# Performance work log

Measured on AMD Instinct MI355X. Metric: run time of the kernel, lower is better.

The kernel has to match this reference:

```python
import jax, jax.numpy as jnp
import numpy as np

B, T, D = 64, 512, 1024   # batch, seq, input_dim
R, O = 1024, 1024          # recurrent_dim, output_dim


def setup_inputs() -> dict:
    key = jax.random.key(0)
    ks = jax.random.split(key, 8)
    s_in = 1.0 / np.sqrt(D)
    s_rec = 1.0 / np.sqrt(R)
    return {
        "x": jax.random.normal(ks[0], (B, T, D), dtype=jnp.float32),
        "Wxh": jax.random.uniform(ks[1], (R, D), jnp.float32, -s_in, s_in),
        "bh": jax.random.uniform(ks[2], (R,), jnp.float32, -s_in, s_in),
        "Whh": jax.random.uniform(ks[3], (R, R), jnp.float32, -s_rec, s_rec),
        "Wxz": jax.random.uniform(ks[4], (R, D), jnp.float32, -s_in, s_in),
        "bz": jax.random.uniform(ks[5], (R,), jnp.float32, -s_in, s_in),
        "Whz": jax.random.uniform(ks[6], (R, R), jnp.float32, -s_rec, s_rec),
        "Wy": jax.random.uniform(ks[7], (O, R), jnp.float32, -s_rec, s_rec),
        "by": jnp.zeros((O,), dtype=jnp.float32),
    }


def reference(x, Wxh, bh, Whh, Wxz, bz, Whz, Wy, by):
    # Original per-step math (note the quirk: h2z output is added to x_t
    # BEFORE x2z):
    #   z  = sigmoid(Wxz @ (x_t + Whz @ h) + bz)
    #   hb = relu(Wxh @ x_t + bh + Whh @ h)
    #   h  = z * h + (1 - z) * hb
    # Precompute all input-side GEMMs in one batched contraction (linearity);
    # fold Wxz@Whz into a single recurrent matrix.
    xh = jnp.einsum('btd,rd->btr', x, Wxh) + bh          # [B,T,R]
    xz = jnp.einsum('btd,rd->btr', x, Wxz) + bz          # [B,T,R]
    Mz = Wxz @ Whz                                        # [R,R]

    def step(h, inp):
        xh_t, xz_t = inp                                  # each [B,R]
        z = jax.nn.sigmoid(xz_t + h @ Mz.T)
        hb = jax.nn.relu(xh_t + h @ Whh.T)
        h = z * h + (1.0 - z) * hb
        return h, None

    h0 = jnp.zeros((x.shape[0], Whh.shape[0]), dtype=x.dtype)
    # scan over time: move T to leading axis
    h_final, _ = jax.lax.scan(
        step, h0, (jnp.swapaxes(xh, 0, 1), jnp.swapaxes(xz, 0, 1)))
    return h_final @ Wy.T + by                            # [B,O]
```

## Files before the change

### kernel.cpp

```cpp
#include <hip/hip_runtime.h>

#define BB 64
#define TT 512
#define DD 1024
#define RR 1024

#define SCAN_BLOCKS 32
#define HS_STRIDE 1032
#define SCAN_LDS_BYTES (64 * HS_STRIDE * 2)

typedef __bf16 bf16x8 __attribute__((ext_vector_type(8)));
typedef float f32x4 __attribute__((ext_vector_type(4)));
typedef unsigned short us4 __attribute__((ext_vector_type(4)));
typedef unsigned int u32x4 __attribute__((ext_vector_type(4)));
typedef unsigned long long u64;

__device__ inline unsigned short f2bf(float f) {
  unsigned int u = __float_as_uint(f);
  u = (u + 0x7fffu + ((u >> 16) & 1u)) >> 16;
  return (unsigned short)u;
}
__device__ inline float bf2f(unsigned short b) {
  return __uint_as_float(((unsigned int)b) << 16);
}

__device__ inline u32x4 ld16_sc(const void* p) {
  u32x4 r;
  asm volatile("global_load_dwordx4 %0, %1, off sc0 sc1"
               : "=v"(r) : "v"(p) : "memory");
  return r;
}

__global__ void k_f2b4(const float* __restrict__ in, unsigned short* __restrict__ out, int n4) {
  int i = blockIdx.x * blockDim.x + threadIdx.x;
  if (i < n4) {
    const float4 v = ((const float4*)in)[i];
    us4 o;
    o.x = f2bf(v.x); o.y = f2bf(v.y); o.z = f2bf(v.z); o.w = f2bf(v.w);
    ((us4*)out)[i] = o;
  }
}

__global__ __launch_bounds__(256) void k_transpose_bf16(
    const float* __restrict__ in, unsigned short* __restrict__ out) {
  __shared__ float tile[32][33];
  const int bx = blockIdx.x * 32, by0 = blockIdx.y * 32;
  const int tx = threadIdx.x, ty = threadIdx.y;
#pragma unroll
  for (int r = 0; r < 32; r += 8)
    tile[ty + r][tx] = in[(size_t)(by0 + ty + r) * 1024 + bx + tx];
  __syncthreads();
#pragma unroll
  for (int r = 0; r < 32; r += 8)
    out[(size_t)(bx + ty + r) * 1024 + by0 + tx] = f2bf(tile[tx][ty + r]);
}

__device__ inline void gload_lds16(const unsigned short* g, unsigned short* l) {
  __builtin_amdgcn_global_load_lds(
      (const __attribute__((address_space(1))) unsigned int*)g,
      (__attribute__((address_space(3))) unsigned int*)l, 16, 0, 0);
}

template <int EPI>
__global__ __launch_bounds__(256) void gemm_bt(
    const unsigned short* __restrict__ A,
    const unsigned short* __restrict__ Bm,
    const float* __restrict__ bias_h,
    const float* __restrict__ bias_z,
    unsigned short* __restrict__ outb, int K) {
  __shared__ __attribute__((aligned(16))) unsigned short As[128 * 32];
  __shared__ __attribute__((aligned(16))) unsigned short Bs[128 * 32];
  const int tid = threadIdx.x;
  const int m0 = blockIdx.y * 128, n0 = blockIdx.x * 128;
  const int lane = tid & 63, wid = tid >> 6;
  const int l16 = lane & 15, quad = lane >> 4;
  const int wm = (wid & 1) * 64, wn = (wid >> 1) * 64;

  f32x4 acc[4][4] = {};

  const int c0 = tid, c1 = 256 + tid;
  const int rowA0 = c0 >> 2, colA0 = (c0 & 3) << 3;
  const int rowA1 = c1 >> 2, colA1 = (c1 & 3) << 3;

  for (int kk = 0; kk < K; kk += 32) {
    __syncthreads();
    gload_lds16(A + (size_t)(m0 + rowA0) * K + kk + colA0, As + c0 * 8);
    gload_lds16(A + (size_t)(m0 + rowA1) * K + kk + colA1, As + c1 * 8);
    gload_lds16(Bm + (size_t)(n0 + rowA0) * K + kk + colA0, Bs + c0 * 8);
    gload_lds16(Bm + (size_t)(n0 + rowA1) * K + kk + colA1, Bs + c1 * 8);
    __syncthreads();
    bf16x8 af[4], bfr[4];
#pragma unroll
    for (int i = 0; i < 4; ++i) {
      af[i] = *(const bf16x8*)&As[(wm + i * 16 + l16) * 32 + quad * 8];
      bfr[i] = *(const bf16x8*)&Bs[(wn + i * 16 + l16) * 32 + quad * 8];
    }
#pragma unroll
    for (int i = 0; i < 4; ++i)
#pragma unroll
      for (int j = 0; j < 4; ++j)
        acc[i][j] = __builtin_amdgcn_mfma_f32_16x16x32_bf16(af[i], bfr[j], acc[i][j], 0, 0, 0);
  }

#pragma unroll
  for (int i = 0; i < 4; ++i) {
#pragma unroll
    for (int j = 0; j < 4; ++j) {
#pragma unroll
      for (int r = 0; r < 4; ++r) {
        const int m = m0 + wm + i * 16 + quad * 4 + r;
        const int n = n0 + wn + j * 16 + l16;
        float v = acc[i][j][r];
        if (EPI == 0) {
          v += (n < 1024) ? bias_h[n] : bias_z[n - 1024];
          const int b = m >> 9;
          const int t = m & 511;
          outb[((size_t)(t * 64 + b) << 11) + n] = f2bf(v);
        } else {
          outb[(size_t)m * 1024 + n] = f2bf(v);
        }
      }
    }
  }
}

__global__ __launch_bounds__(1024) void scan_out_k(
    const unsigned short* __restrict__ xhz,
    const unsigned short* __restrict__ Wrec,
    const unsigned short* __restrict__ Wyb,
    const float* __restrict__ by,
    unsigned short* __restrict__ hb0, unsigned short* __restrict__ hb1,
    unsigned int* __restrict__ flags,
    float* __restrict__ out) {
  extern __shared__ char smem[];
  unsigned short* hs = (unsigned short*)smem;
  float* red = (float*)smem;

  const int tid = threadIdx.x, g = blockIdx.x;
  const int lane = tid & 63, wid = tid >> 6;
  const int l16 = lane & 15, quad = lane >> 4;
  const int ks = wid >> 2, nsub = wid & 3;
  const int kw = ks * 256;
  const int i0 = g * 32;

  const int bcol = (nsub < 2) ? (i0 + nsub * 16 + l16)
                              : (1024 + i0 + (nsub - 2) * 16 + l16);
  const unsigned short* Bb = Wrec + (size_t)bcol * 1024 + kw + quad * 8;
  bf16x8 bfr[8];
#pragma unroll
  for (int s = 0; s < 8; ++s) bfr[s] = *(const bf16x8*)(Bb + s * 32);

  const int sr = tid >> 4;
  const int su = tid & 15;
  const unsigned short* gsrc_base0 = hb0 + sr * 1024 + su * 8;
  const unsigned short* gsrc_base1 = hb1 + sr * 1024 + su * 8;
  unsigned short* ldst = hs + sr * HS_STRIDE + su * 8;

  const int eb = tid >> 4, ej = (tid & 15) * 2;
  float hold0 = 0.0f, hold1 = 0.0f;

  const unsigned short* hbc = hb0;
  unsigned short* hbn = hb1;
  const unsigned short* gsrc = gsrc_base0;

  for (int tt = 0; tt < TT; ++tt) {
    u32x4 tmp[8];
#pragma unroll
    for (int c = 0; c < 8; ++c)
      tmp[c] = ld16_sc((const char*)gsrc + c * 256);
    const size_t xrow = ((size_t)(tt * 64 + eb)) << 11;
    const unsigned int xh2 = *(const unsigned int*)(xhz + xrow + i0 + ej);
    const unsigned int xz2 = *(const unsigned int*)(xhz + xrow + 1024 + i0 + ej);
    asm volatile("s_waitcnt vmcnt(0)" ::: "memory");
#pragma unroll
    for (int c = 0; c < 8; ++c)
      *(u32x4*)(ldst + c * 128) = tmp[c];
    __syncthreads();

    f32x4 acc[4] = {};
#pragma unroll
    for (int s = 0; s < 8; ++s) {
#pragma unroll
      for (int mt = 0; mt < 4; ++mt) {
        const bf16x8 afr = *(const bf16x8*)(hs + (mt * 16 + l16) * HS_STRIDE + kw + s * 32 + quad * 8);
        acc[mt] = __builtin_amdgcn_mfma_f32_16x16x32_bf16(afr, bfr[s], acc[mt], 0, 0, 0);
      }
    }
    __syncthreads();

#pragma unroll
    for (int mt = 0; mt < 4; ++mt)
#pragma unroll
      for (int r = 0; r < 4; ++r)
        red[(size_t)(ks * 64 + mt * 16 + quad * 4 + r) * 68 + nsub * 16 + l16] = acc[mt][r];
    __syncthreads();

    float ph0 = 0.f, ph1 = 0.f, pz0 = 0.f, pz1 = 0.f;
#pragma unroll
    for (int w = 0; w < 4; ++w) {
      const float* rb = red + (size_t)(w * 64 + eb) * 68;
      ph0 += rb[ej]; ph1 += rb[ej + 1];
      pz0 += rb[32 + ej]; pz1 += rb[32 + ej + 1];
    }
    {
      const float xh0 = bf2f((unsigned short)(xh2 & 0xffff));
      const float xh1 = bf2f((unsigned short)(xh2 >> 16));
      const float xz0 = bf2f((unsigned short)(xz2 & 0xffff));
      const float xz1 = bf2f((unsigned short)(xz2 >> 16));
      const float z0 = 1.0f / (1.0f + __expf(-(xz0 + pz0)));
      const float z1 = 1.0f / (1.0f + __expf(-(xz1 + pz1)));
      const float hb_0 = fmaxf(xh0 + ph0, 0.0f);
      const float hb_1 = fmaxf(xh1 + ph1, 0.0f);
      hold0 = z0 * hold0 + (1.0f - z0) * hb_0;
      hold1 = z1 * hold1 + (1.0f - z1) * hb_1;
      const unsigned int pk = (unsigned int)f2bf(hold0) | ((unsigned int)f2bf(hold1) << 16);
      __hip_atomic_store((unsigned int*)(hbn + eb * 1024 + i0 + ej), pk,
                         __ATOMIC_RELAXED, __HIP_MEMORY_SCOPE_AGENT);
    }

    __syncthreads();
    if (tid == 0)
      __hip_atomic_store(&flags[g], (unsigned int)(tt + 1),
                         __ATOMIC_RELAXED, __HIP_MEMORY_SCOPE_AGENT);
    if (tid < 64) {
      const unsigned int tgt = (unsigned int)(tt + 1);
      unsigned int v;
      do {
        v = __hip_atomic_load(&flags[tid & 31], __ATOMIC_RELAXED, __HIP_MEMORY_SCOPE_AGENT);
      } while (__any(v < tgt));
    }
    __syncthreads();

    const unsigned short* tc = hbc; hbc = hbn; hbn = (unsigned short*)tc;
    gsrc = (tt & 1) ? gsrc_base0 : gsrc_base1;
  }

  {
    u32x4 tmp[8];
#pragma unroll
    for (int c = 0; c < 8; ++c)
      tmp[c] = ld16_sc((const char*)(hbc + sr * 1024 + su * 8) + c * 256);
    asm volatile("s_waitcnt vmcnt(0)" ::: "memory");
#pragma unroll
    for (int c = 0; c < 8; ++c)
      *(u32x4*)(ldst + c * 128) = tmp[c];
  }
  __syncthreads();

  if (nsub < 2) {
    const int ocol = i0 + nsub * 16 + l16;
    const unsigned short* Byb = Wyb + (size_t)ocol * 1024 + kw + quad * 8;
    f32x4 acc[4] = {};
#pragma unroll
    for (int s = 0; s < 8; ++s) {
      const bf16x8 byf = *(const bf16x8*)(Byb + s * 32);
#pragma unroll
      for (int mt = 0; mt < 4; ++mt) {
        const bf16x8 afr = *(const bf16x8*)(hs + (mt * 16 + l16) * HS_STRIDE + kw + s * 32 + quad * 8);
        acc[mt] = __builtin_amdgcn_mfma_f32_16x16x32_bf16(afr, byf, acc[mt], 0, 0, 0);
      }
    }
    __syncthreads();
#pragma unroll
    for (int mt = 0; mt < 4; ++mt)
#pragma unroll
      for (int r = 0; r < 4; ++r)
        red[(size_t)(ks * 64 + mt * 16 + quad * 4 + r) * 68 + nsub * 16 + l16] = acc[mt][r];
  } else {
    __syncthreads();
  }
  __syncthreads();

  {
    float o0 = by[i0 + ej], o1 = by[i0 + ej + 1];
#pragma unroll
    for (int w = 0; w < 4; ++w) {
      const float* rb = red + (size_t)(w * 64 + eb) * 68;
      o0 += rb[ej]; o1 += rb[ej + 1];
    }
    float2 ov; ov.x = o0; ov.y = o1;
    *(float2*)(out + (size_t)eb * 1024 + i0 + ej) = ov;
  }
}

extern "C" void kernel_launch(void* const* d_in, const int* in_sizes, int n_in,
                              void* d_out, int out_size, void* d_ws, size_t ws_size,
                              hipStream_t stream) {
  const float* x = (const float*)d_in[0];
  const float* Wxh = (const float*)d_in[1];
  const float* bh = (const float*)d_in[2];
  const float* Whh = (const float*)d_in[3];
  const float* Wxz = (const float*)d_in[4];
  const float* bz = (const float*)d_in[5];
  const float* Whz = (const float*)d_in[6];
  const float* Wy = (const float*)d_in[7];
  const float* by = (const float*)d_in[8];
  float* out = (float*)d_out;

  char* ws = (char*)d_ws;
  size_t off = 0;
  auto alloc = [&](size_t bytes) -> void* {
    void* p = ws + off;
    off += (bytes + 255) & ~(size_t)255;
    return p;
  };
  const size_t nX = (size_t)BB * TT * DD;
  unsigned short* xb = (unsigned short*)alloc(nX * 2);
  unsigned short* Wcat = (unsigned short*)alloc((size_t)2048 * 1024 * 2);
  unsigned short* WhzT = (unsigned short*)alloc((size_t)1024 * 1024 * 2);
  unsigned short* Wrec = (unsigned short*)alloc((size_t)2048 * 1024 * 2);
  unsigned short* Wyb = (unsigned short*)alloc((size_t)1024 * 1024 * 2);
  unsigned short* xhz = (unsigned short*)alloc((size_t)TT * BB * 2048 * 2);
  unsigned short* hb0 = (unsigned short*)alloc((size_t)BB * RR * 2);
  unsigned short* hb1 = (unsigned short*)alloc((size_t)BB * RR * 2);
  unsigned int* flags = (unsigned int*)alloc(1024);

  hipMemsetAsync(hb0, 0, (size_t)BB * RR * 2, stream);
  hipMemsetAsync(flags, 0, 1024, stream);

  k_f2b4<<<dim3((unsigned)(nX / 4 / 256)), 256, 0, stream>>>(x, xb, (int)(nX / 4));
  k_f2b4<<<dim3(1024), 256, 0, stream>>>(Wxh, Wcat, 262144);
  k_f2b4<<<dim3(1024), 256, 0, stream>>>(Wxz, Wcat + 1024 * 1024, 262144);
  k_f2b4<<<dim3(1024), 256, 0, stream>>>(Whh, Wrec, 262144);
  k_f2b4<<<dim3(1024), 256, 0, stream>>>(Wy, Wyb, 262144);
  k_transpose_bf16<<<dim3(32, 32), dim3(32, 8), 0, stream>>>(Whz, WhzT);

  gemm_bt<1><<<dim3(8, 8), 256, 0, stream>>>(Wcat + 1024 * 1024, WhzT, nullptr, nullptr,
                                             Wrec + (size_t)1024 * 1024, 1024);
  gemm_bt<0><<<dim3(16, 256), 256, 0, stream>>>(xb, Wcat, bh, bz, xhz, 1024);

  hipFuncSetAttribute((const void*)scan_out_k,
                      hipFuncAttributeMaxDynamicSharedMemorySize, SCAN_LDS_BYTES);
  const unsigned short* xhz_c = xhz;
  const unsigned short* Wrec_c = Wrec;
  const unsigned short* Wyb_c = Wyb;
  const float* by_c = by;
  void* kargs[] = {(void*)&xhz_c, (void*)&Wrec_c, (void*)&Wyb_c, (void*)&by_c,
                   (void*)&hb0, (void*)&hb1, (void*)&flags, (void*)&out};
  hipLaunchCooperativeKernel((void*)scan_out_k, dim3(SCAN_BLOCKS), dim3(1024),
                             kargs, SCAN_LDS_BYTES, stream);
}
```

Measured before the change: 3.379 ms.

## Restructure recurrent scan to 64 blocks with LDS-resident weights and direct-register h loads

The persistent scan kernel moves from 32 blocks of 1024 threads to 64 blocks of 256 threads. Each block keeps its 16 h-columns and 16 z-columns of the recurrent weights in LDS, and each wave streams its 16 batch rows of h straight from global memory into MFMA operand registers, with staged waitcnt pipelining. This removes the LDS staging of h, the cross-wave K-split reduction and several block barriers per step. The flag wait moves to the start of the next step so the xhz loads overlap it. In exchange, each block reads the full h from global every step, and 64 blocks now take part in the grid-wide flag sync.

```diff
diff --git a/kernel.cpp b/kernel.cpp
--- a/kernel.cpp
+++ b/kernel.cpp
@@ -5,15 +5,16 @@
 #define DD 1024
 #define RR 1024
 
-#define SCAN_BLOCKS 32
-#define HS_STRIDE 1032
-#define SCAN_LDS_BYTES (64 * HS_STRIDE * 2)
+#define NBLK 64
+#define WST 1032
+#define SCAN_LDS_BYTES (64 * WST * 2)
+#define SCRATCH_OFF (32 * WST * 2)
 
 typedef __bf16 bf16x8 __attribute__((ext_vector_type(8)));
 typedef float f32x4 __attribute__((ext_vector_type(4)));
 typedef unsigned short us4 __attribute__((ext_vector_type(4)));
 typedef unsigned int u32x4 __attribute__((ext_vector_type(4)));
-typedef unsigned long long u64;
+typedef unsigned int u32x2 __attribute__((ext_vector_type(2)));
 
 __device__ inline unsigned short f2bf(float f) {
   unsigned int u = __float_as_uint(f);
@@ -29,6 +30,15 @@
   asm volatile("global_load_dwordx4 %0, %1, off sc0 sc1"
                : "=v"(r) : "v"(p) : "memory");
   return r;
+}
+__device__ inline void st8_sc(void* p, u32x2 v) {
+  asm volatile("global_store_dwordx2 %0, %1, off sc0 sc1"
+               :: "v"(p), "v"(v) : "memory");
+}
+
+__device__ inline void issue8(u32x4* d, const char* base) {
+#pragma unroll
+  for (int i = 0; i < 8; ++i) d[i] = ld16_sc(base + (size_t)i * 64);
 }
 
 __global__ void k_f2b4(const float* __restrict__ in, unsigned short* __restrict__ out, int n4) {
@@ -124,7 +134,7 @@
   }
 }
 
-__global__ __launch_bounds__(1024) void scan_out_k(
+__global__ __launch_bounds__(256, 1) void scan_out_k(
     const unsigned short* __restrict__ xhz,
     const unsigned short* __restrict__ Wrec,
     const unsigned short* __restrict__ Wyb,
@@ -133,153 +143,139 @@
     unsigned int* __restrict__ flags,
     float* __restrict__ out) {
   extern __shared__ char smem[];
-  unsigned short* hs = (unsigned short*)smem;
-  float* red = (float*)smem;
+  unsigned short* wlds = (unsigned short*)smem;
 
   const int tid = threadIdx.x, g = blockIdx.x;
-  const int lane = tid & 63, wid = tid >> 6;
+  const int lane = tid & 63, rg = tid >> 6;
   const int l16 = lane & 15, quad = lane >> 4;
-  const int ks = wid >> 2, nsub = wid & 3;
-  const int kw = ks * 256;
-  const int i0 = g * 32;
-
-  const int bcol = (nsub < 2) ? (i0 + nsub * 16 + l16)
-                              : (1024 + i0 + (nsub - 2) * 16 + l16);
-  const unsigned short* Bb = Wrec + (size_t)bcol * 1024 + kw + quad * 8;
-  bf16x8 bfr[8];
-#pragma unroll
-  for (int s = 0; s < 8; ++s) bfr[s] = *(const bf16x8*)(Bb + s * 32);
-
-  const int sr = tid >> 4;
-  const int su = tid & 15;
-  const unsigned short* gsrc_base0 = hb0 + sr * 1024 + su * 8;
-  const unsigned short* gsrc_base1 = hb1 + sr * 1024 + su * 8;
-  unsigned short* ldst = hs + sr * HS_STRIDE + su * 8;
-
-  const int eb = tid >> 4, ej = (tid & 15) * 2;
-  float hold0 = 0.0f, hold1 = 0.0f;
-
-  const unsigned short* hbc = hb0;
-  unsigned short* hbn = hb1;
-  const unsigned short* gsrc = gsrc_base0;
+
+  {
+    const int row = tid >> 3, seg = tid & 7;
+    const unsigned short* src = (row < 16)
+        ? Wrec + ((size_t)(g * 16 + row) << 10)
+        : Wrec + ((size_t)(1024 + g * 16 + (row - 16)) << 10);
+    src += seg * 128;
+    unsigned short* dst = wlds + row * WST + seg * 128;
+#pragma unroll
+    for (int i = 0; i < 16; ++i)
+      *(u32x4*)(dst + i * 8) = *(const u32x4*)(src + i * 8);
+  }
+  __syncthreads();
+
+  const size_t abase = ((size_t)(rg * 16 + l16) << 11) + quad * 16;
+  const unsigned short* wh = wlds + (size_t)l16 * WST + quad * 8;
+  const unsigned short* wz = wlds + (size_t)(16 + l16) * WST + quad * 8;
+  char* scratch = smem + SCRATCH_OFF + rg * 512;
+  const int b_ew = rg * 16 + quad * 4;
+  const int col = g * 16 + l16;
+  const size_t pub_off = ((size_t)(rg * 16 + (lane >> 2)) << 11) + g * 32 + (lane & 3) * 8;
+
+  float hold[4] = {0.f, 0.f, 0.f, 0.f};
 
   for (int tt = 0; tt < TT; ++tt) {
-    u32x4 tmp[8];
-#pragma unroll
-    for (int c = 0; c < 8; ++c)
-      tmp[c] = ld16_sc((const char*)gsrc + c * 256);
-    const size_t xrow = ((size_t)(tt * 64 + eb)) << 11;
-    const unsigned int xh2 = *(const unsigned int*)(xhz + xrow + i0 + ej);
-    const unsigned int xz2 = *(const unsigned int*)(xhz + xrow + 1024 + i0 + ej);
+    unsigned short xh[4], xz[4];
+    {
+      const size_t xb = ((size_t)(tt * 64 + b_ew)) << 11;
+#pragma unroll
+      for (int r = 0; r < 4; ++r) {
+        xh[r] = xhz[xb + ((size_t)r << 11) + col];
+        xz[r] = xhz[xb + ((size_t)r << 11) + 1024 + col];
+      }
+    }
+    {
+      const unsigned int tgt = (unsigned int)tt;
+      unsigned int v;
+      do {
+        v = __hip_atomic_load(&flags[lane], __ATOMIC_RELAXED, __HIP_MEMORY_SCOPE_AGENT);
+      } while (__any(v < tgt));
+    }
+
+    const char* hb = (tt & 1) ? (const char*)hb1 : (const char*)hb0;
+    unsigned short* hd = (tt & 1) ? hb0 : hb1;
+
+    u32x4 tbuf[4][8];
+    issue8(tbuf[0], hb + abase);
+    issue8(tbuf[1], hb + abase + 512);
+    f32x4 acc0 = {0.f, 0.f, 0.f, 0.f};
+    f32x4 acc1 = {0.f, 0.f, 0.f, 0.f};
+#pragma unroll
+    for (int c = 0; c < 4; ++c) {
+      if (c < 2) issue8(tbuf[c + 2], hb + abase + (size_t)(c + 2) * 512);
+      if (c < 2)       asm volatile("s_waitcnt vmcnt(16)" ::: "memory");
+      else if (c == 2) asm volatile("s_waitcnt vmcnt(8)" ::: "memory");
+      else             asm volatile("s_waitcnt vmcnt(0)" ::: "memory");
+      __builtin_amdgcn_sched_barrier(0);
+#pragma unroll
+      for (int i = 0; i < 8; ++i) {
+        const int kk = c * 8 + i;
+        const bf16x8 a = __builtin_bit_cast(bf16x8, tbuf[c][i]);
+        acc0 = __builtin_amdgcn_mfma_f32_16x16x32_bf16(a, *(const bf16x8*)(wh + kk * 32), acc0, 0, 0, 0);
+        acc1 = __builtin_amdgcn_mfma_f32_16x16x32_bf16(a, *(const bf16x8*)(wz + kk * 32), acc1, 0, 0, 0);
+      }
+    }
+
+    unsigned short hp[4];
+#pragma unroll
+    for (int r = 0; r < 4; ++r) {
+      const float xhf = bf2f(xh[r]), xzf = bf2f(xz[r]);
+      const float z = 1.0f / (1.0f + __expf(-(xzf + acc1[r])));
+      const float hbv = fmaxf(xhf + acc0[r], 0.0f);
+      hold[r] = z * hold[r] + (1.0f - z) * hbv;
+      hp[r] = f2bf(hold[r]);
+    }
+#pragma unroll
+    for (int r = 0; r < 4; ++r)
+      ((unsigned short*)scratch)[(quad * 4 + r) * 16 + l16] = hp[r];
+    asm volatile("s_waitcnt lgkmcnt(0)" ::: "memory");
+    __builtin_amdgcn_sched_barrier(0);
+    const u32x2 pv = *(const u32x2*)(scratch + lane * 8);
+    st8_sc((char*)hd + pub_off, pv);
+
     asm volatile("s_waitcnt vmcnt(0)" ::: "memory");
-#pragma unroll
-    for (int c = 0; c < 8; ++c)
-      *(u32x4*)(ldst + c * 128) = tmp[c];
-    __syncthreads();
-
-    f32x4 acc[4] = {};
-#pragma unroll
-    for (int s = 0; s < 8; ++s) {
-#pragma unroll
-      for (int mt = 0; mt < 4; ++mt) {
-        const bf16x8 afr = *(const bf16x8*)(hs + (mt * 16 + l16) * HS_STRIDE + kw + s * 32 + quad * 8);
-        acc[mt] = __builtin_amdgcn_mfma_f32_16x16x32_bf16(afr, bfr[s], acc[mt], 0, 0, 0);
-      }
-    }
-    __syncthreads();
-
-#pragma unroll
-    for (int mt = 0; mt < 4; ++mt)
-#pragma unroll
-      for (int r = 0; r < 4; ++r)
-        red[(size_t)(ks * 64 + mt * 16 + quad * 4 + r) * 68 + nsub * 16 + l16] = acc[mt][r];
-    __syncthreads();
-
-    float ph0 = 0.f, ph1 = 0.f, pz0 = 0.f, pz1 = 0.f;
-#pragma unroll
-    for (int w = 0; w < 4; ++w) {
-      const float* rb = red + (size_t)(w * 64 + eb) * 68;
-      ph0 += rb[ej]; ph1 += rb[ej + 1];
-      pz0 += rb[32 + ej]; pz1 += rb[32 + ej + 1];
-    }
-    {
-      const float xh0 = bf2f((unsigned short)(xh2 & 0xffff));
-      const float xh1 = bf2f((unsigned short)(xh2 >> 16));
-      const float xz0 = bf2f((unsigned short)(xz2 & 0xffff));
-      const float xz1 = bf2f((unsigned short)(xz2 >> 16));
-      const float z0 = 1.0f / (1.0f + __expf(-(xz0 + pz0)));
-      const float z1 = 1.0f / (1.0f + __expf(-(xz1 + pz1)));
-      const float hb_0 = fmaxf(xh0 + ph0, 0.0f);
-      const float hb_1 = fmaxf(xh1 + ph1, 0.0f);
-      hold0 = z0 * hold0 + (1.0f - z0) * hb_0;
-      hold1 = z1 * hold1 + (1.0f - z1) * hb_1;
-      const unsigned int pk = (unsigned int)f2bf(hold0) | ((unsigned int)f2bf(hold1) << 16);
-      __hip_atomic_store((unsigned int*)(hbn + eb * 1024 + i0 + ej), pk,
-                         __ATOMIC_RELAXED, __HIP_MEMORY_SCOPE_AGENT);
-    }
-
     __syncthreads();
     if (tid == 0)
       __hip_atomic_store(&flags[g], (unsigned int)(tt + 1),
                          __ATOMIC_RELAXED, __HIP_MEMORY_SCOPE_AGENT);
-    if (tid < 64) {
-      const unsigned int tgt = (unsigned int)(tt + 1);
-      unsigned int v;
-      do {
-        v = __hip_atomic_load(&flags[tid & 31], __ATOMIC_RELAXED, __HIP_MEMORY_SCOPE_AGENT);
-      } while (__any(v < tgt));
-    }
-    __syncthreads();
-
-    const unsigned short* tc = hbc; hbc = hbn; hbn = (unsigned short*)tc;
-    gsrc = (tt & 1) ? gsrc_base0 : gsrc_base1;
   }
 
   {
-    u32x4 tmp[8];
-#pragma unroll
-    for (int c = 0; c < 8; ++c)
-      tmp[c] = ld16_sc((const char*)(hbc + sr * 1024 + su * 8) + c * 256);
-    asm volatile("s_waitcnt vmcnt(0)" ::: "memory");
-#pragma unroll
-    for (int c = 0; c < 8; ++c)
-      *(u32x4*)(ldst + c * 128) = tmp[c];
+    unsigned int v;
+    do {
+      v = __hip_atomic_load(&flags[lane], __ATOMIC_RELAXED, __HIP_MEMORY_SCOPE_AGENT);
+    } while (__any(v < (unsigned int)TT));
   }
   __syncthreads();
-
-  if (nsub < 2) {
-    const int ocol = i0 + nsub * 16 + l16;
-    const unsigned short* Byb = Wyb + (size_t)ocol * 1024 + kw + quad * 8;
-    f32x4 acc[4] = {};
-#pragma unroll
-    for (int s = 0; s < 8; ++s) {
-      const bf16x8 byf = *(const bf16x8*)(Byb + s * 32);
-#pragma unroll
-      for (int mt = 0; mt < 4; ++mt) {
-        const bf16x8 afr = *(const bf16x8*)(hs + (mt * 16 + l16) * HS_STRIDE + kw + s * 32 + quad * 8);
-        acc[mt] = __builtin_amdgcn_mfma_f32_16x16x32_bf16(afr, byf, acc[mt], 0, 0, 0);
-      }
-    }
-    __syncthreads();
-#pragma unroll
-    for (int mt = 0; mt < 4; ++mt)
-#pragma unroll
-      for (int r = 0; r < 4; ++r)
-        red[(size_t)(ks * 64 + mt * 16 + quad * 4 + r) * 68 + nsub * 16 + l16] = acc[mt][r];
-  } else {
-    __syncthreads();
+  {
+    const char* hfin = (const char*)hb0;
+    const int row = tid >> 2, seg = tid & 3;
+    const size_t gb = ((size_t)row << 11) + seg * 512;
+    unsigned short* dst = wlds + (size_t)row * WST + seg * 256;
+#pragma unroll
+    for (int c = 0; c < 4; ++c) {
+      u32x4 t4[8];
+#pragma unroll
+      for (int i = 0; i < 8; ++i) t4[i] = ld16_sc(hfin + gb + (size_t)(c * 8 + i) * 16);
+      asm volatile("s_waitcnt vmcnt(0)" ::: "memory");
+      __builtin_amdgcn_sched_barrier(0);
+#pragma unroll
+      for (int i = 0; i < 8; ++i) *(u32x4*)(dst + (c * 8 + i) * 8) = t4[i];
+    }
   }
   __syncthreads();
-
   {
-    float o0 = by[i0 + ej], o1 = by[i0 + ej + 1];
-#pragma unroll
-    for (int w = 0; w < 4; ++w) {
-      const float* rb = red + (size_t)(w * 64 + eb) * 68;
-      o0 += rb[ej]; o1 += rb[ej + 1];
-    }
-    float2 ov; ov.x = o0; ov.y = o1;
-    *(float2*)(out + (size_t)eb * 1024 + i0 + ej) = ov;
+    const unsigned short* a_l = wlds + (size_t)(rg * 16 + l16) * WST + quad * 8;
+    const unsigned short* byw = Wyb + ((size_t)col << 10) + quad * 8;
+    f32x4 acc = {0.f, 0.f, 0.f, 0.f};
+#pragma unroll
+    for (int kk = 0; kk < 32; ++kk) {
+      const bf16x8 a = *(const bf16x8*)(a_l + kk * 32);
+      const bf16x8 b = *(const bf16x8*)(byw + kk * 32);
+      acc = __builtin_amdgcn_mfma_f32_16x16x32_bf16(a, b, acc, 0, 0, 0);
+    }
+    const float bias = by[col];
+#pragma unroll
+    for (int r = 0; r < 4; ++r)
+      out[((size_t)(rg * 16 + quad * 4 + r) << 10) + col] = acc[r] + bias;
   }
 }
 
@@ -337,6 +333,6 @@
   const float* by_c = by;
   void* kargs[] = {(void*)&xhz_c, (void*)&Wrec_c, (void*)&Wyb_c, (void*)&by_c,
                    (void*)&hb0, (void*)&hb1, (void*)&flags, (void*)&out};
-  hipLaunchCooperativeKernel((void*)scan_out_k, dim3(SCAN_BLOCKS), dim3(1024),
+  hipLaunchCooperativeKernel((void*)scan_out_k, dim3(NBLK), dim3(256),
                              kargs, SCAN_LDS_BYTES, stream);
 }
```

Result: slower. 3.885 ms (+14.9%).

## Replace flag-based grid barrier with sentinel-poisoned 4-slot hidden-state ring

Applied to the files above, without the earlier changes.

Drops the per-step global flag barrier, which needed two __syncthreads, a flag store and a spin on all 32 flags. Each block now reads the previous hidden state from a 4-slot ring and spins on the data itself until no 0xFFFFFFFF sentinel remains. As it publishes its slice for the current step, each block re-poisons the slot two steps ahead. This removes a full grid barrier per timestep, at the cost of extra stores and a sentinel check, and it relies on a real bf16 pair never equalling the sentinel and on the ring depth preventing overwrite races.

```diff
diff --git a/kernel.cpp b/kernel.cpp
--- a/kernel.cpp
+++ b/kernel.cpp
@@ -8,12 +8,12 @@
 #define SCAN_BLOCKS 32
 #define HS_STRIDE 1032
 #define SCAN_LDS_BYTES (64 * HS_STRIDE * 2)
+#define SLOT_BYTES (BB * RR * 2)
 
 typedef __bf16 bf16x8 __attribute__((ext_vector_type(8)));
 typedef float f32x4 __attribute__((ext_vector_type(4)));
 typedef unsigned short us4 __attribute__((ext_vector_type(4)));
 typedef unsigned int u32x4 __attribute__((ext_vector_type(4)));
-typedef unsigned long long u64;
 
 __device__ inline unsigned short f2bf(float f) {
   unsigned int u = __float_as_uint(f);
@@ -29,6 +29,10 @@
   asm volatile("global_load_dwordx4 %0, %1, off sc0 sc1"
                : "=v"(r) : "v"(p) : "memory");
   return r;
+}
+__device__ inline void st4_sc(void* p, unsigned int v) {
+  asm volatile("global_store_dword %0, %1, off sc0 sc1"
+               :: "v"(p), "v"(v) : "memory");
 }
 
 __global__ void k_f2b4(const float* __restrict__ in, unsigned short* __restrict__ out, int n4) {
@@ -129,8 +133,7 @@
     const unsigned short* __restrict__ Wrec,
     const unsigned short* __restrict__ Wyb,
     const float* __restrict__ by,
-    unsigned short* __restrict__ hb0, unsigned short* __restrict__ hb1,
-    unsigned int* __restrict__ flags,
+    unsigned short* __restrict__ hring,
     float* __restrict__ out) {
   extern __shared__ char smem[];
   unsigned short* hs = (unsigned short*)smem;
@@ -152,26 +155,51 @@
 
   const int sr = tid >> 4;
   const int su = tid & 15;
-  const unsigned short* gsrc_base0 = hb0 + sr * 1024 + su * 8;
-  const unsigned short* gsrc_base1 = hb1 + sr * 1024 + su * 8;
+  const size_t srow = (size_t)sr * 2048 + su * 16;
   unsigned short* ldst = hs + sr * HS_STRIDE + su * 8;
 
   const int eb = tid >> 4, ej = (tid & 15) * 2;
+  const size_t pub_elem = (size_t)eb * 1024 + i0 + ej;
   float hold0 = 0.0f, hold1 = 0.0f;
 
-  const unsigned short* hbc = hb0;
-  unsigned short* hbn = hb1;
-  const unsigned short* gsrc = gsrc_base0;
-
   for (int tt = 0; tt < TT; ++tt) {
+    const char* src = (const char*)hring + (size_t)((tt + 3) & 3) * SLOT_BYTES;
+    char* dst = (char*)hring + (size_t)(tt & 3) * SLOT_BYTES;
+    char* poi = (char*)hring + (size_t)((tt + 2) & 3) * SLOT_BYTES;
+
     u32x4 tmp[8];
 #pragma unroll
     for (int c = 0; c < 8; ++c)
-      tmp[c] = ld16_sc((const char*)gsrc + c * 256);
+      tmp[c] = ld16_sc(src + srow + c * 256);
     const size_t xrow = ((size_t)(tt * 64 + eb)) << 11;
     const unsigned int xh2 = *(const unsigned int*)(xhz + xrow + i0 + ej);
     const unsigned int xz2 = *(const unsigned int*)(xhz + xrow + 1024 + i0 + ej);
     asm volatile("s_waitcnt vmcnt(0)" ::: "memory");
+    __builtin_amdgcn_sched_barrier(0);
+
+    unsigned int bad = 0;
+#pragma unroll
+    for (int c = 0; c < 8; ++c) {
+      bool b = false;
+#pragma unroll
+      for (int i = 0; i < 4; ++i) b = b || (tmp[c][i] == 0xFFFFFFFFu);
+      if (b) bad |= (1u << c);
+    }
+    while (__any(bad != 0)) {
+#pragma unroll
+      for (int c = 0; c < 8; ++c)
+        if (bad & (1u << c)) tmp[c] = ld16_sc(src + srow + c * 256);
+      asm volatile("s_waitcnt vmcnt(0)" ::: "memory");
+      __builtin_amdgcn_sched_barrier(0);
+      bad = 0;
+#pragma unroll
+      for (int c = 0; c < 8; ++c) {
+        bool b = false;
+#pragma unroll
+        for (int i = 0; i < 4; ++i) b = b || (tmp[c][i] == 0xFFFFFFFFu);
+        if (b) bad |= (1u << c);
+      }
+    }
 #pragma unroll
     for (int c = 0; c < 8; ++c)
       *(u32x4*)(ldst + c * 128) = tmp[c];
@@ -214,33 +242,43 @@
       hold0 = z0 * hold0 + (1.0f - z0) * hb_0;
       hold1 = z1 * hold1 + (1.0f - z1) * hb_1;
       const unsigned int pk = (unsigned int)f2bf(hold0) | ((unsigned int)f2bf(hold1) << 16);
-      __hip_atomic_store((unsigned int*)(hbn + eb * 1024 + i0 + ej), pk,
-                         __ATOMIC_RELAXED, __HIP_MEMORY_SCOPE_AGENT);
-    }
-
-    __syncthreads();
-    if (tid == 0)
-      __hip_atomic_store(&flags[g], (unsigned int)(tt + 1),
-                         __ATOMIC_RELAXED, __HIP_MEMORY_SCOPE_AGENT);
-    if (tid < 64) {
-      const unsigned int tgt = (unsigned int)(tt + 1);
-      unsigned int v;
-      do {
-        v = __hip_atomic_load(&flags[tid & 31], __ATOMIC_RELAXED, __HIP_MEMORY_SCOPE_AGENT);
-      } while (__any(v < tgt));
-    }
-    __syncthreads();
-
-    const unsigned short* tc = hbc; hbc = hbn; hbn = (unsigned short*)tc;
-    gsrc = (tt & 1) ? gsrc_base0 : gsrc_base1;
+      st4_sc(dst + pub_elem * 2, pk);
+      st4_sc(poi + pub_elem * 2, 0xFFFFFFFFu);
+    }
+    __syncthreads();
   }
 
   {
+    const char* src = (const char*)hring + (size_t)3 * SLOT_BYTES;
     u32x4 tmp[8];
 #pragma unroll
     for (int c = 0; c < 8; ++c)
-      tmp[c] = ld16_sc((const char*)(hbc + sr * 1024 + su * 8) + c * 256);
+      tmp[c] = ld16_sc(src + srow + c * 256);
     asm volatile("s_waitcnt vmcnt(0)" ::: "memory");
+    __builtin_amdgcn_sched_barrier(0);
+    unsigned int bad = 0;
+#pragma unroll
+    for (int c = 0; c < 8; ++c) {
+      bool b = false;
+#pragma unroll
+      for (int i = 0; i < 4; ++i) b = b || (tmp[c][i] == 0xFFFFFFFFu);
+      if (b) bad |= (1u << c);
+    }
+    while (__any(bad != 0)) {
+#pragma unroll
+      for (int c = 0; c < 8; ++c)
+        if (bad & (1u << c)) tmp[c] = ld16_sc(src + srow + c * 256);
+      asm volatile("s_waitcnt vmcnt(0)" ::: "memory");
+      __builtin_amdgcn_sched_barrier(0);
+      bad = 0;
+#pragma unroll
+      for (int c = 0; c < 8; ++c) {
+        bool b = false;
+#pragma unroll
+        for (int i = 0; i < 4; ++i) b = b || (tmp[c][i] == 0xFFFFFFFFu);
+        if (b) bad |= (1u << c);
+      }
+    }
 #pragma unroll
     for (int c = 0; c < 8; ++c)
       *(u32x4*)(ldst + c * 128) = tmp[c];
@@ -311,12 +349,10 @@
   unsigned short* Wrec = (unsigned short*)alloc((size_t)2048 * 1024 * 2);
   unsigned short* Wyb = (unsigned short*)alloc((size_t)1024 * 1024 * 2);
   unsigned short* xhz = (unsigned short*)alloc((size_t)TT * BB * 2048 * 2);
-  unsigned short* hb0 = (unsigned short*)alloc((size_t)BB * RR * 2);
-  unsigned short* hb1 = (unsigned short*)alloc((size_t)BB * RR * 2);
-  unsigned int* flags = (unsigned int*)alloc(1024);
-
-  hipMemsetAsync(hb0, 0, (size_t)BB * RR * 2, stream);
-  hipMemsetAsync(flags, 0, 1024, stream);
+  unsigned short* hring = (unsigned short*)alloc((size_t)4 * SLOT_BYTES);
+
+  hipMemsetAsync(hring, 0xFF, (size_t)3 * SLOT_BYTES, stream);
+  hipMemsetAsync((char*)hring + (size_t)3 * SLOT_BYTES, 0, SLOT_BYTES, stream);
 
   k_f2b4<<<dim3((unsigned)(nX / 4 / 256)), 256, 0, stream>>>(x, xb, (int)(nX / 4));
   k_f2b4<<<dim3(1024), 256, 0, stream>>>(Wxh, Wcat, 262144);
@@ -335,8 +371,9 @@
   const unsigned short* Wrec_c = Wrec;
   const unsigned short* Wyb_c = Wyb;
   const float* by_c = by;
+  unsigned short* hring_c = hring;
   void* kargs[] = {(void*)&xhz_c, (void*)&Wrec_c, (void*)&Wyb_c, (void*)&by_c,
-                   (void*)&hb0, (void*)&hb1, (void*)&flags, (void*)&out};
+                   (void*)&hring_c, (void*)&out};
   hipLaunchCooperativeKernel((void*)scan_out_k, dim3(SCAN_BLOCKS), dim3(1024),
                              kargs, SCAN_LDS_BYTES, stream);
 }
```

Result: slower. 3.529 ms (+4.4%).

## Load recurrent state fragments directly from global into MFMA registers, halve block size

Applied to the files above, without the earlier changes.

The scan kernel no longer stages the full hidden state into LDS each step. Each wave now loads its A fragments straight from global memory through a 3-deep software-pipelined register buffer, and the xhz loads are interleaved into that pipeline. Blocks shrink to 512 threads, with each wave computing two N tiles. This removes one LDS round trip and a __syncthreads per timestep, at the cost of more redundant global/L2 reads of h per block and more registers. The final output GEMM now reads h from hb0, which relies on TT being even so the last step wrote hb0.

```diff
diff --git a/kernel.cpp b/kernel.cpp
--- a/kernel.cpp
+++ b/kernel.cpp
@@ -6,13 +6,14 @@
 #define RR 1024
 
 #define SCAN_BLOCKS 32
-#define HS_STRIDE 1032
-#define SCAN_LDS_BYTES (64 * HS_STRIDE * 2)
+#define RED_STRIDE 68
+#define SCAN_LDS_BYTES (4 * 64 * RED_STRIDE * 4)
 
 typedef __bf16 bf16x8 __attribute__((ext_vector_type(8)));
 typedef float f32x4 __attribute__((ext_vector_type(4)));
 typedef unsigned short us4 __attribute__((ext_vector_type(4)));
 typedef unsigned int u32x4 __attribute__((ext_vector_type(4)));
+typedef unsigned int u32x2 __attribute__((ext_vector_type(2)));
 typedef unsigned long long u64;
 
 __device__ inline unsigned short f2bf(float f) {
@@ -28,6 +29,11 @@
   u32x4 r;
   asm volatile("global_load_dwordx4 %0, %1, off sc0 sc1"
                : "=v"(r) : "v"(p) : "memory");
+  return r;
+}
+__device__ inline u32x2 ld8_g(const void* p) {
+  u32x2 r;
+  asm volatile("global_load_dwordx2 %0, %1, off" : "=v"(r) : "v"(p) : "memory");
   return r;
 }
 
@@ -124,7 +130,7 @@
   }
 }
 
-__global__ __launch_bounds__(1024) void scan_out_k(
+__global__ __launch_bounds__(512, 2) void scan_out_k(
     const unsigned short* __restrict__ xhz,
     const unsigned short* __restrict__ Wrec,
     const unsigned short* __restrict__ Wyb,
@@ -132,91 +138,105 @@
     unsigned short* __restrict__ hb0, unsigned short* __restrict__ hb1,
     unsigned int* __restrict__ flags,
     float* __restrict__ out) {
-  extern __shared__ char smem[];
-  unsigned short* hs = (unsigned short*)smem;
-  float* red = (float*)smem;
+  extern __shared__ float red[];
 
   const int tid = threadIdx.x, g = blockIdx.x;
   const int lane = tid & 63, wid = tid >> 6;
   const int l16 = lane & 15, quad = lane >> 4;
-  const int ks = wid >> 2, nsub = wid & 3;
+  const int ks = wid >> 1, ng = wid & 1;
   const int kw = ks * 256;
   const int i0 = g * 32;
 
-  const int bcol = (nsub < 2) ? (i0 + nsub * 16 + l16)
-                              : (1024 + i0 + (nsub - 2) * 16 + l16);
-  const unsigned short* Bb = Wrec + (size_t)bcol * 1024 + kw + quad * 8;
-  bf16x8 bfr[8];
-#pragma unroll
-  for (int s = 0; s < 8; ++s) bfr[s] = *(const bf16x8*)(Bb + s * 32);
-
-  const int sr = tid >> 4;
-  const int su = tid & 15;
-  const unsigned short* gsrc_base0 = hb0 + sr * 1024 + su * 8;
-  const unsigned short* gsrc_base1 = hb1 + sr * 1024 + su * 8;
-  unsigned short* ldst = hs + sr * HS_STRIDE + su * 8;
-
-  const int eb = tid >> 4, ej = (tid & 15) * 2;
-  float hold0 = 0.0f, hold1 = 0.0f;
-
-  const unsigned short* hbc = hb0;
-  unsigned short* hbn = hb1;
-  const unsigned short* gsrc = gsrc_base0;
+  bf16x8 bfr[2][8];
+#pragma unroll
+  for (int j = 0; j < 2; ++j) {
+    const int nt = ng * 2 + j;
+    const int bcol = (nt < 2) ? (i0 + nt * 16 + l16)
+                              : (1024 + i0 + (nt - 2) * 16 + l16);
+    const unsigned short* Bb = Wrec + (size_t)bcol * 1024 + kw + quad * 8;
+#pragma unroll
+    for (int s = 0; s < 8; ++s) bfr[j][s] = *(const bf16x8*)(Bb + s * 32);
+  }
+
+  const size_t abase = (size_t)l16 * 2048 + (size_t)(kw + quad * 8) * 2;
+
+  const int eb = tid >> 3, ej = (tid & 7) * 4;
+  float hold[4] = {0.f, 0.f, 0.f, 0.f};
 
   for (int tt = 0; tt < TT; ++tt) {
-    u32x4 tmp[8];
-#pragma unroll
-    for (int c = 0; c < 8; ++c)
-      tmp[c] = ld16_sc((const char*)gsrc + c * 256);
-    const size_t xrow = ((size_t)(tt * 64 + eb)) << 11;
-    const unsigned int xh2 = *(const unsigned int*)(xhz + xrow + i0 + ej);
-    const unsigned int xz2 = *(const unsigned int*)(xhz + xrow + 1024 + i0 + ej);
+    const char* hbc = (tt & 1) ? (const char*)hb1 : (const char*)hb0;
+    unsigned short* hbn = (tt & 1) ? hb0 : hb1;
+
+    f32x4 acc[4][2] = {};
+    u32x4 tA[3][4];
+    u32x2 xh2 = {}, xz2 = {};
+#pragma unroll
+    for (int mt = 0; mt < 4; ++mt)
+      tA[0][mt] = ld16_sc(hbc + abase + mt * 32768);
+#pragma unroll
+    for (int mt = 0; mt < 4; ++mt)
+      tA[1][mt] = ld16_sc(hbc + abase + mt * 32768 + 64);
+#pragma unroll
+    for (int s = 0; s < 8; ++s) {
+      if (s < 6) {
+#pragma unroll
+        for (int mt = 0; mt < 4; ++mt)
+          tA[(s + 2) % 3][mt] = ld16_sc(hbc + abase + mt * 32768 + (s + 2) * 64);
+      }
+      if (s == 6) {
+        const char* xp = (const char*)xhz +
+            (((((size_t)tt * 64 + eb)) << 11) + i0 + ej) * 2;
+        xh2 = ld8_g(xp);
+        xz2 = ld8_g(xp + 2048);
+      }
+      if (s < 6)       asm volatile("s_waitcnt vmcnt(8)" ::: "memory");
+      else if (s == 6) asm volatile("s_waitcnt vmcnt(6)" ::: "memory");
+      else             asm volatile("s_waitcnt vmcnt(2)" ::: "memory");
+      __builtin_amdgcn_sched_barrier(0);
+#pragma unroll
+      for (int mt = 0; mt < 4; ++mt) {
+        const bf16x8 a = __builtin_bit_cast(bf16x8, tA[s % 3][mt]);
+        acc[mt][0] = __builtin_amdgcn_mfma_f32_16x16x32_bf16(a, bfr[0][s], acc[mt][0], 0, 0, 0);
+        acc[mt][1] = __builtin_amdgcn_mfma_f32_16x16x32_bf16(a, bfr[1][s], acc[mt][1], 0, 0, 0);
+      }
+    }
+
+#pragma unroll
+    for (int mt = 0; mt < 4; ++mt)
+#pragma unroll
+      for (int j = 0; j < 2; ++j)
+#pragma unroll
+        for (int r = 0; r < 4; ++r)
+          red[(size_t)(ks * 64 + mt * 16 + quad * 4 + r) * RED_STRIDE +
+              (ng * 2 + j) * 16 + l16] = acc[mt][j][r];
+    __syncthreads();
+
     asm volatile("s_waitcnt vmcnt(0)" ::: "memory");
-#pragma unroll
-    for (int c = 0; c < 8; ++c)
-      *(u32x4*)(ldst + c * 128) = tmp[c];
-    __syncthreads();
-
-    f32x4 acc[4] = {};
-#pragma unroll
-    for (int s = 0; s < 8; ++s) {
-#pragma unroll
-      for (int mt = 0; mt < 4; ++mt) {
-        const bf16x8 afr = *(const bf16x8*)(hs + (mt * 16 + l16) * HS_STRIDE + kw + s * 32 + quad * 8);
-        acc[mt] = __builtin_amdgcn_mfma_f32_16x16x32_bf16(afr, bfr[s], acc[mt], 0, 0, 0);
-      }
-    }
-    __syncthreads();
-
-#pragma unroll
-    for (int mt = 0; mt < 4; ++mt)
-#pragma unroll
-      for (int r = 0; r < 4; ++r)
-        red[(size_t)(ks * 64 + mt * 16 + quad * 4 + r) * 68 + nsub * 16 + l16] = acc[mt][r];
-    __syncthreads();
-
-    float ph0 = 0.f, ph1 = 0.f, pz0 = 0.f, pz1 = 0.f;
+    __builtin_amdgcn_sched_barrier(0);
+    float ph[4] = {}, pz[4] = {};
 #pragma unroll
     for (int w = 0; w < 4; ++w) {
-      const float* rb = red + (size_t)(w * 64 + eb) * 68;
-      ph0 += rb[ej]; ph1 += rb[ej + 1];
-      pz0 += rb[32 + ej]; pz1 += rb[32 + ej + 1];
-    }
-    {
-      const float xh0 = bf2f((unsigned short)(xh2 & 0xffff));
-      const float xh1 = bf2f((unsigned short)(xh2 >> 16));
-      const float xz0 = bf2f((unsigned short)(xz2 & 0xffff));
-      const float xz1 = bf2f((unsigned short)(xz2 >> 16));
-      const float z0 = 1.0f / (1.0f + __expf(-(xz0 + pz0)));
-      const float z1 = 1.0f / (1.0f + __expf(-(xz1 + pz1)));
-      const float hb_0 = fmaxf(xh0 + ph0, 0.0f);
-      const float hb_1 = fmaxf(xh1 + ph1, 0.0f);
-      hold0 = z0 * hold0 + (1.0f - z0) * hb_0;
-      hold1 = z1 * hold1 + (1.0f - z1) * hb_1;
-      const unsigned int pk = (unsigned int)f2bf(hold0) | ((unsigned int)f2bf(hold1) << 16);
-      __hip_atomic_store((unsigned int*)(hbn + eb * 1024 + i0 + ej), pk,
-                         __ATOMIC_RELAXED, __HIP_MEMORY_SCOPE_AGENT);
-    }
+      const float* rb = red + (size_t)(w * 64 + eb) * RED_STRIDE;
+#pragma unroll
+      for (int r = 0; r < 4; ++r) {
+        ph[r] += rb[ej + r];
+        pz[r] += rb[32 + ej + r];
+      }
+    }
+    unsigned short hp[4];
+#pragma unroll
+    for (int r = 0; r < 4; ++r) {
+      const unsigned int xw = xh2[r >> 1], zw = xz2[r >> 1];
+      const float xhf = bf2f((unsigned short)((r & 1) ? (xw >> 16) : (xw & 0xffff)));
+      const float xzf = bf2f((unsigned short)((r & 1) ? (zw >> 16) : (zw & 0xffff)));
+      const float z = 1.0f / (1.0f + __expf(-(xzf + pz[r])));
+      const float hbv = fmaxf(xhf + ph[r], 0.0f);
+      hold[r] = z * hold[r] + (1.0f - z) * hbv;
+      hp[r] = f2bf(hold[r]);
+    }
+    const u64 pk = (u64)hp[0] | ((u64)hp[1] << 16) | ((u64)hp[2] << 32) | ((u64)hp[3] << 48);
+    __hip_atomic_store((u64*)(hbn + (size_t)eb * 1024 + i0 + ej), pk,
+                       __ATOMIC_RELAXED, __HIP_MEMORY_SCOPE_AGENT);
 
     __syncthreads();
     if (tid == 0)
@@ -230,56 +250,60 @@
       } while (__any(v < tgt));
     }
     __syncthreads();
-
-    const unsigned short* tc = hbc; hbc = hbn; hbn = (unsigned short*)tc;
-    gsrc = (tt & 1) ? gsrc_base0 : gsrc_base1;
   }
 
   {
-    u32x4 tmp[8];
-#pragma unroll
-    for (int c = 0; c < 8; ++c)
-      tmp[c] = ld16_sc((const char*)(hbc + sr * 1024 + su * 8) + c * 256);
-    asm volatile("s_waitcnt vmcnt(0)" ::: "memory");
-#pragma unroll
-    for (int c = 0; c < 8; ++c)
-      *(u32x4*)(ldst + c * 128) = tmp[c];
+    const int ocol = i0 + ng * 16 + l16;
+    const unsigned short* Byb = Wyb + (size_t)ocol * 1024 + kw + quad * 8;
+    bf16x8 byf[8];
+#pragma unroll
+    for (int s = 0; s < 8; ++s) byf[s] = *(const bf16x8*)(Byb + s * 32);
+
+    f32x4 acc[4] = {};
+    u32x4 tA[3][4];
+#pragma unroll
+    for (int mt = 0; mt < 4; ++mt)
+      tA[0][mt] = ld16_sc((const char*)hb0 + abase + mt * 32768);
+#pragma unroll
+    for (int mt = 0; mt < 4; ++mt)
+      tA[1][mt] = ld16_sc((const char*)hb0 + abase + mt * 32768 + 64);
+#pragma unroll
+    for (int s = 0; s < 8; ++s) {
+      if (s < 6) {
+#pragma unroll
+        for (int mt = 0; mt < 4; ++mt)
+          tA[(s + 2) % 3][mt] = ld16_sc((const char*)hb0 + abase + mt * 32768 + (s + 2) * 64);
+      }
+      if (s < 6)       asm volatile("s_waitcnt vmcnt(8)" ::: "memory");
+      else if (s == 6) asm volatile("s_waitcnt vmcnt(4)" ::: "memory");
+      else             asm volatile("s_waitcnt vmcnt(0)" ::: "memory");
+      __builtin_amdgcn_sched_barrier(0);
+#pragma unroll
+      for (int mt = 0; mt < 4; ++mt) {
+        const bf16x8 a = __builtin_bit_cast(bf16x8, tA[s % 3][mt]);
+        acc[mt] = __builtin_amdgcn_mfma_f32_16x16x32_bf16(a, byf[s], acc[mt], 0, 0, 0);
+      }
+    }
+#pragma unroll
+    for (int mt = 0; mt < 4; ++mt)
+#pragma unroll
+      for (int r = 0; r < 4; ++r)
+        red[(size_t)(ks * 64 + mt * 16 + quad * 4 + r) * RED_STRIDE +
+            ng * 16 + l16] = acc[mt][r];
   }
   __syncthreads();
-
-  if (nsub < 2) {
-    const int ocol = i0 + nsub * 16 + l16;
-    const unsigned short* Byb = Wyb + (size_t)ocol * 1024 + kw + quad * 8;
-    f32x4 acc[4] = {};
-#pragma unroll
-    for (int s = 0; s < 8; ++s) {
-      const bf16x8 byf = *(const bf16x8*)(Byb + s * 32);
-#pragma unroll
-      for (int mt = 0; mt < 4; ++mt) {
-        const bf16x8 afr = *(const bf16x8*)(hs + (mt * 16 + l16) * HS_STRIDE + kw + s * 32 + quad * 8);
-        acc[mt] = __builtin_amdgcn_mfma_f32_16x16x32_bf16(afr, byf, acc[mt], 0, 0, 0);
-      }
-    }
-    __syncthreads();
-#pragma unroll
-    for (int mt = 0; mt < 4; ++mt)
-#pragma unroll
-      for (int r = 0; r < 4; ++r)
-        red[(size_t)(ks * 64 + mt * 16 + quad * 4 + r) * 68 + nsub * 16 + l16] = acc[mt][r];
-  } else {
-    __syncthreads();
-  }
-  __syncthreads();
-
   {
-    float o0 = by[i0 + ej], o1 = by[i0 + ej + 1];
+    float o[4];
+#pragma unroll
+    for (int r = 0; r < 4; ++r) o[r] = by[i0 + ej + r];
 #pragma unroll
     for (int w = 0; w < 4; ++w) {
-      const float* rb = red + (size_t)(w * 64 + eb) * 68;
-      o0 += rb[ej]; o1 += rb[ej + 1];
-    }
-    float2 ov; ov.x = o0; ov.y = o1;
-    *(float2*)(out + (size_t)eb * 1024 + i0 + ej) = ov;
+      const float* rb = red + (size_t)(w * 64 + eb) * RED_STRIDE;
+#pragma unroll
+      for (int r = 0; r < 4; ++r) o[r] += rb[ej + r];
+    }
+    float4 ov; ov.x = o[0]; ov.y = o[1]; ov.z = o[2]; ov.w = o[3];
+    *(float4*)(out + (size_t)eb * 1024 + i0 + ej) = ov;
   }
 }
 
@@ -337,6 +361,6 @@
   const float* by_c = by;
   void* kargs[] = {(void*)&xhz_c, (void*)&Wrec_c, (void*)&Wyb_c, (void*)&by_c,
                    (void*)&hb0, (void*)&hb1, (void*)&flags, (void*)&out};
-  hipLaunchCooperativeKernel((void*)scan_out_k, dim3(SCAN_BLOCKS), dim3(1024),
+  hipLaunchCooperativeKernel((void*)scan_out_k, dim3(SCAN_BLOCKS), dim3(512),
                              kargs, SCAN_LDS_BYTES, stream);
 }
```

Result: slower. 5.467 ms (+61.8%).
